# Kernel tuning notes

Measured on AMD Instinct MI355X. Metric: run time of the kernel, lower is better.

The kernel has to match this reference:

```python
import jax, jax.numpy as jnp
import numpy as np

N = 50000
E = 800000
D = 256   # output_channel_dim
K = 32
L = 4     # num_of_layers


def setup_inputs() -> dict:
    key = jax.random.key(0)
    ks = jax.random.split(key, 10)
    x = jax.random.normal(ks[0], (N, 1), dtype=jnp.float32)
    edge_index = jax.random.randint(ks[1], (2, E), 0, N, dtype=jnp.int64)
    edge_attr = jax.random.uniform(ks[2], (E,), dtype=jnp.float32)
    # GGNN per-layer propagation weights (L, D, D)
    weight = jax.random.normal(ks[3], (L, D, D), dtype=jnp.float32) / np.sqrt(D)
    # GRUCell params (torch layout: [r|z|n] stacked along first dim)
    w_ih = jax.random.normal(ks[4], (3 * D, D), dtype=jnp.float32) / np.sqrt(D)
    w_hh = jax.random.normal(ks[5], (3 * D, D), dtype=jnp.float32) / np.sqrt(D)
    b_ih = jax.random.normal(ks[6], (3 * D,), dtype=jnp.float32) * 0.01
    b_hh = jax.random.normal(ks[7], (3 * D,), dtype=jnp.float32) * 0.01
    # readout Linear(D, K)
    w_ro = jax.random.normal(ks[8], (D, K), dtype=jnp.float32) / np.sqrt(D)
    b_ro = jax.random.normal(ks[9], (K,), dtype=jnp.float32) * 0.01
    return {"x": x, "edge_index": edge_index, "edge_attr": edge_attr,
            "weight": weight, "w_ih": w_ih, "w_hh": w_hh,
            "b_ih": b_ih, "b_hh": b_hh, "w_ro": w_ro, "b_ro": b_ro}


def _gru_cell(m, h, w_ih, w_hh, b_ih, b_hh):
    # torch.nn.GRUCell math; gates stacked [r|z|n]
    gi = m @ w_ih.T + b_ih   # (N, 3D)
    gh = h @ w_hh.T + b_hh   # (N, 3D)
    i_r, i_z, i_n = jnp.split(gi, 3, axis=-1)
    h_r, h_z, h_n = jnp.split(gh, 3, axis=-1)
    r = jax.nn.sigmoid(i_r + h_r)
    z = jax.nn.sigmoid(i_z + h_z)
    n = jnp.tanh(i_n + r * h_n)
    return (1.0 - z) * n + z * h


def reference(x, edge_index, edge_attr, weight, w_ih, w_hh, b_ih, b_hh, w_ro, b_ro):
    src, dst = edge_index[0], edge_index[1]
    n_nodes, d = x.shape[0], weight.shape[-1]
    # pad input features with zeros up to out_channels
    h = jnp.concatenate([x, jnp.zeros((n_nodes, d - x.shape[-1]), x.dtype)], axis=-1)
    for i in range(weight.shape[0]):
        m = h @ weight[i]                                    # (N, D)
        msg = edge_attr[:, None] * m[src]                    # (E, D)
        agg = jax.ops.segment_sum(msg, dst, num_segments=n_nodes)  # (N, D)
        h = _gru_cell(agg, h, w_ih, w_hh, b_ih, b_hh)
    logits = h @ w_ro + b_ro                                 # (N, K)
    return jax.nn.softmax(logits, axis=-1)
```

## Files before the change

kernel.cpp:

```cpp
#include <hip/hip_runtime.h>

#define D 256
#define K_OUT 32
#define L_LAYERS 4
#define NPAD 50048

typedef __attribute__((ext_vector_type(8))) short bf16x8;
typedef __attribute__((ext_vector_type(4))) float f32x4;
typedef __attribute__((address_space(3))) unsigned int lds_u32;
typedef const __attribute__((address_space(1))) unsigned int glb_u32;

__device__ __forceinline__ float sigm(float v) { return 1.f / (1.f + __expf(-v)); }
__device__ __forceinline__ unsigned short f2bf(float f) {
    unsigned u = __float_as_uint(f);
    u = u + 0x7fffu + ((u >> 16) & 1u);
    return (unsigned short)(u >> 16);
}
__device__ __forceinline__ float bf2f(unsigned short s) {
    return __uint_as_float(((unsigned)s) << 16);
}
__device__ __forceinline__ void gload16(const unsigned short* g, unsigned short* l) {
    __builtin_amdgcn_global_load_lds((glb_u32*)g, (lds_u32*)l, 16, 0, 0);
}

__device__ __forceinline__ void frag_addr(int f, int bm, int bnd, int lane,
                                          unsigned& off, bool& isA, bool& isG2) {
    if (f < 8) {
        off = (unsigned)(bm + f * 16 + (lane & 15)) * 1024u + ((lane >> 4) << 3);
        isA = true; isG2 = false;
    } else if (f < 16) {
        off = (unsigned)(bm + (f - 8) * 16 + (lane & 15)) * 1024u + 512u + ((lane >> 4) << 3);
        isA = true; isG2 = false;
    } else if (f < 28) {
        int q = f - 16; int gs = q >> 2; int df = q & 3;
        off = (unsigned)(gs * 256 + bnd + df * 16 + (lane & 15)) * 1024u + ((lane >> 4) << 3);
        isA = false; isG2 = (gs == 2);
    } else {
        int q = f - 28; int gs = q >> 2; int df = q & 3;
        off = (unsigned)(gs * 256 + bnd + df * 16 + (lane & 15)) * 1024u + 512u + ((lane >> 4) << 3);
        isA = false; isG2 = (gs == 2);
    }
}

__global__ __launch_bounds__(256) void hist_kernel(const int* __restrict__ dst,
                                                   int* __restrict__ cnt, int E) {
    int idx = blockIdx.x * blockDim.x + threadIdx.x;
    for (int e = idx; e < E; e += gridDim.x * blockDim.x)
        atomicAdd(&cnt[dst[e]], 1);
}

__global__ __launch_bounds__(1024) void scan_kernel(const int* __restrict__ cnt,
                                                    int* __restrict__ rowptr,
                                                    int* __restrict__ cursor, int n) {
    __shared__ int sdata[1024];
    int t = threadIdx.x;
    int chunk = (n + 1023) / 1024;
    int start = t * chunk;
    int end = start + chunk; if (end > n) end = n;
    int s = 0;
    for (int i = start; i < end; i++) s += cnt[i];
    sdata[t] = s;
    __syncthreads();
    for (int off = 1; off < 1024; off <<= 1) {
        int v = (t >= off) ? sdata[t - off] : 0;
        __syncthreads();
        sdata[t] += v;
        __syncthreads();
    }
    int base = sdata[t] - s;
    for (int i = start; i < end; i++) {
        rowptr[i] = base;
        cursor[i] = base;
        base += cnt[i];
    }
    if (end == n && start <= n) rowptr[n] = base;
}

__global__ __launch_bounds__(256) void reorder_kernel(const int* __restrict__ src,
                                                      const int* __restrict__ dst,
                                                      const float* __restrict__ ea,
                                                      int* __restrict__ cursor,
                                                      int* __restrict__ esrc,
                                                      float* __restrict__ eval, int E) {
    int idx = blockIdx.x * blockDim.x + threadIdx.x;
    for (int e = idx; e < E; e += gridDim.x * blockDim.x) {
        int slot = atomicAdd(&cursor[dst[e]], 1);
        esrc[slot] = src[e];
        eval[slot] = ea[e];
    }
}

__global__ __launch_bounds__(256) void prep_wih_kernel(const float* __restrict__ weight,
                                                       const float* __restrict__ w_ih,
                                                       float* __restrict__ P) {
    int l = blockIdx.z;
    const float* A = weight + (size_t)l * D * D;
    float* Cdst = P + (size_t)l * 256 * 768;
    __shared__ float As[32][64 + 4];
    __shared__ float Bs[32][64 + 4];
    int tid = threadIdx.x;
    int tx = tid & 15, ty = tid >> 4;
    int bk = blockIdx.x * 64;
    int bn = blockIdx.y * 64;
    float acc[4][4] = {};
    for (int jb = 0; jb < D; jb += 32) {
        #pragma unroll
        for (int i = 0; i < 2; i++) {
            int lin = tid + i * 256;
            int row = lin >> 3;
            int c4 = (lin & 7) << 2;
            float4 v = *(const float4*)&A[(size_t)(bk + row) * D + jb + c4];
            As[c4+0][row]=v.x; As[c4+1][row]=v.y; As[c4+2][row]=v.z; As[c4+3][row]=v.w;
            float4 w = *(const float4*)&w_ih[(size_t)(bn + row) * D + jb + c4];
            Bs[c4+0][row]=w.x; Bs[c4+1][row]=w.y; Bs[c4+2][row]=w.z; Bs[c4+3][row]=w.w;
        }
        __syncthreads();
        #pragma unroll
        for (int jj = 0; jj < 32; jj++) {
            float a[4], b[4];
            *(float4*)a = *(const float4*)&As[jj][ty*4];
            *(float4*)b = *(const float4*)&Bs[jj][tx*4];
            #pragma unroll
            for (int i = 0; i < 4; i++)
                #pragma unroll
                for (int j = 0; j < 4; j++)
                    acc[i][j] += a[i] * b[j];
        }
        __syncthreads();
    }
    #pragma unroll
    for (int i = 0; i < 4; i++)
        *(float4*)&Cdst[(size_t)(bk + ty*4 + i) * 768 + bn + tx*4] =
            make_float4(acc[i][0], acc[i][1], acc[i][2], acc[i][3]);
}

__global__ __launch_bounds__(256) void pack_bt2_kernel(const float* __restrict__ P,
                                                       const float* __restrict__ w_hh,
                                                       unsigned short* __restrict__ BT2) {
    long long idx = (long long)blockIdx.x * 256 + threadIdx.x;
    int l = (int)(idx >> 20);
    int rem = (int)(idx & 1048575);
    int c = rem >> 10;
    int k2 = rem & 1023;
    int g = c >> 8, d = c & 255;
    int k = k2 & 511;
    float val;
    if (k < 256) {
        val = (g == 0) ? P[(size_t)l * 196608 + (size_t)k * 768 + d]
            : (g == 1) ? P[(size_t)l * 196608 + (size_t)k * 768 + 256 + d]
            : (g == 2) ? P[(size_t)l * 196608 + (size_t)k * 768 + 512 + d]
            : 0.f;
    } else {
        int kk = k - 256;
        val = (g == 0) ? w_hh[(size_t)d * D + kk]
            : (g == 1) ? w_hh[(size_t)(256 + d) * D + kk]
            : (g == 3) ? w_hh[(size_t)(512 + d) * D + kk]
            : 0.f;
    }
    unsigned short hi = f2bf(val);
    BT2[idx] = (k2 < 512) ? hi : f2bf(val - bf2f(hi));
}

__global__ __launch_bounds__(256) void sgather_kernel(const float* __restrict__ x,
                                                      const int* __restrict__ rowptr,
                                                      const int* __restrict__ esrc,
                                                      const float* __restrict__ eval,
                                                      float* __restrict__ sx, int n) {
    int node = blockIdx.x * blockDim.x + threadIdx.x;
    if (node >= n) return;
    float s = 0.f;
    int end = rowptr[node + 1];
    for (int e = rowptr[node]; e < end; e++) s += eval[e] * x[esrc[e]];
    sx[node] = s;
}

__global__ __launch_bounds__(256) void layer0_kernel(const float* __restrict__ x,
                                                     const float* __restrict__ sx,
                                                     const float* __restrict__ P0,
                                                     const float* __restrict__ w_hh,
                                                     const float* __restrict__ b_ih,
                                                     const float* __restrict__ b_hh,
                                                     float* __restrict__ hout, int M) {
    int node = blockIdx.x * 4 + (threadIdx.x >> 6);
    if (node >= M) return;
    int d0 = (threadIdx.x & 63) * 4;
    float sxn = sx[node], xn = x[node];
    float4 r0 = *(const float4*)&P0[d0];
    float4 z0 = *(const float4*)&P0[256 + d0];
    float4 n0 = *(const float4*)&P0[512 + d0];
    float r1[4], z1[4], n1[4];
    #pragma unroll
    for (int j = 0; j < 4; j++) {
        r1[j] = w_hh[(size_t)(d0 + j) * D];
        z1[j] = w_hh[(size_t)(256 + d0 + j) * D];
        n1[j] = w_hh[(size_t)(512 + d0 + j) * D];
    }
    float4 bir = *(const float4*)&b_ih[d0];
    float4 biz = *(const float4*)&b_ih[256 + d0];
    float4 bin = *(const float4*)&b_ih[512 + d0];
    float4 bhr = *(const float4*)&b_hh[d0];
    float4 bhz = *(const float4*)&b_hh[256 + d0];
    float4 bhn = *(const float4*)&b_hh[512 + d0];
    float rr[4] = {sxn*r0.x + xn*r1[0] + bir.x + bhr.x, sxn*r0.y + xn*r1[1] + bir.y + bhr.y,
                   sxn*r0.z + xn*r1[2] + bir.z + bhr.z, sxn*r0.w + xn*r1[3] + bir.w + bhr.w};
    float zz[4] = {sxn*z0.x + xn*z1[0] + biz.x + bhz.x, sxn*z0.y + xn*z1[1] + biz.y + bhz.y,
                   sxn*z0.z + xn*z1[2] + biz.z + bhz.z, sxn*z0.w + xn*z1[3] + biz.w + bhz.w};
    float ni[4] = {sxn*n0.x + bin.x, sxn*n0.y + bin.y, sxn*n0.z + bin.z, sxn*n0.w + bin.w};
    float nh[4] = {xn*n1[0] + bhn.x, xn*n1[1] + bhn.y, xn*n1[2] + bhn.z, xn*n1[3] + bhn.w};
    float o[4];
    #pragma unroll
    for (int j = 0; j < 4; j++) {
        float r = sigm(rr[j]);
        float z = sigm(zz[j]);
        float nn = tanhf(ni[j] + r * nh[j]);
        float hp = (d0 + j == 0) ? xn : 0.f;
        o[j] = (1.f - z) * nn + z * hp;
    }
    *(float4*)&hout[(size_t)node * D + d0] = make_float4(o[0], o[1], o[2], o[3]);
}

__global__ __launch_bounds__(256) void gather_bf_kernel(const float* __restrict__ h,
                                                        const int* __restrict__ rowptr,
                                                        const int* __restrict__ esrc,
                                                        const float* __restrict__ eval,
                                                        unsigned short* __restrict__ A2, int n) {
    int node = (blockIdx.x * 256 + threadIdx.x) >> 6;
    int lane = threadIdx.x & 63;
    if (node >= n) return;
    int beg = rowptr[node], end = rowptr[node + 1];
    float4 acc = make_float4(0.f, 0.f, 0.f, 0.f);
    for (int e = beg; e < end; e++) {
        int s = esrc[e];
        float a = eval[e];
        float4 v = *(const float4*)&h[(size_t)s * D + lane * 4];
        acc.x += a * v.x; acc.y += a * v.y; acc.z += a * v.z; acc.w += a * v.w;
    }
    ushort4 hi = make_ushort4(f2bf(acc.x), f2bf(acc.y), f2bf(acc.z), f2bf(acc.w));
    ushort4 lo = make_ushort4(f2bf(acc.x - bf2f(hi.x)), f2bf(acc.y - bf2f(hi.y)),
                              f2bf(acc.z - bf2f(hi.z)), f2bf(acc.w - bf2f(hi.w)));
    *(ushort4*)&A2[(size_t)node * 1024 + lane * 4] = hi;
    *(ushort4*)&A2[(size_t)node * 1024 + 512 + lane * 4] = lo;
    float4 hv = *(const float4*)&h[(size_t)node * D + lane * 4];
    ushort4 hh = make_ushort4(f2bf(hv.x), f2bf(hv.y), f2bf(hv.z), f2bf(hv.w));
    ushort4 hl = make_ushort4(f2bf(hv.x - bf2f(hh.x)), f2bf(hv.y - bf2f(hh.y)),
                              f2bf(hv.z - bf2f(hh.z)), f2bf(hv.w - bf2f(hh.w)));
    *(ushort4*)&A2[(size_t)node * 1024 + 256 + lane * 4] = hh;
    *(ushort4*)&A2[(size_t)node * 1024 + 768 + lane * 4] = hl;
}

__global__ __launch_bounds__(256, 2) void gru_mfma_kernel(const unsigned short* __restrict__ A2,
                                                          const unsigned short* __restrict__ BT2,
                                                          const float* __restrict__ b_ih,
                                                          const float* __restrict__ b_hh,
                                                          float* __restrict__ h, int M) {
    __shared__ unsigned short sm[2][20480];
    int tid = threadIdx.x;
    int lane = tid & 63;
    int wid = tid >> 6;
    int wr = wid >> 1, wc = wid & 1;

    int bid = blockIdx.x;
    int g, by;
    if (bid < 1536) {
        int ch = bid >> 5;
        int rem = bid & 31;
        g = ch * 8 + (rem & 7);
        by = rem >> 3;
    } else {
        int r = bid - 1536;
        g = 384 + (r >> 2);
        by = r & 3;
    }
    int bm = g * 128;
    int bnd = by * 64;

    unsigned g0off[5], g1off[5];
    int slot0[5], slot1[5];
    bool g0A[5], g0G2[5], g1A[5], g1G2[5];
    #pragma unroll
    for (int i = 0; i < 5; i++) {
        int idx = wid * 5 + i;
        int f0 = (idx < 8) ? idx : idx + 8;
        int f1 = (idx < 8) ? idx + 8 : idx + 20;
        frag_addr(f0, bm, bnd, lane, g0off[i], g0A[i], g0G2[i]);
        frag_addr(f1, bm, bnd, lane, g1off[i], g1A[i], g1G2[i]);
        slot0[i] = f0; slot1[i] = f1;
    }

    f32x4 acc[4][8];
    #pragma unroll
    for (int i = 0; i < 4; i++)
        #pragma unroll
        for (int j = 0; j < 8; j++)
            acc[i][j] = (f32x4){0.f, 0.f, 0.f, 0.f};

    bf16x8 ah[4], al[4], bh[6], bl[6];

#define STAGE_H0(C_, B_)                                                           \
    { _Pragma("unroll")                                                            \
      for (int i = 0; i < 5; i++) {                                                \
        const unsigned short* gp = (g0A[i] ? A2 : BT2) + g0off[i]                  \
            + (C_) * 32 + ((g0G2[i] && (C_) >= 8) ? 262144u : 0u);                 \
        gload16(gp, &sm[B_][slot0[i] * 512]);                                      \
      } }
#define STAGE_H1(C_, B_)                                                           \
    { _Pragma("unroll")                                                            \
      for (int i = 0; i < 5; i++) {                                                \
        const unsigned short* gp = (g1A[i] ? A2 : BT2) + g1off[i]                  \
            + (C_) * 32 + ((g1G2[i] && (C_) >= 8) ? 262144u : 0u);                 \
        gload16(gp, &sm[B_][slot1[i] * 512]);                                      \
      } }

#define KBODY(C_, NIOFF_)                                                          \
    {   int cur = (C_) & 1;                                                        \
        asm volatile("s_waitcnt vmcnt(5)" ::: "memory");                           \
        __builtin_amdgcn_sched_barrier(0);                                         \
        __builtin_amdgcn_s_barrier();                                              \
        if ((C_) < 15) { STAGE_H0((C_) + 1, cur ^ 1); STAGE_H1((C_) + 1, cur ^ 1); } \
        _Pragma("unroll")                                                          \
        for (int m = 0; m < 4; m++)                                                \
            ah[m] = *(const bf16x8*)&sm[cur][(wr * 4 + m) * 512 + lane * 8];       \
        _Pragma("unroll")                                                          \
        for (int j = 0; j < 6; j++) {                                              \
            int fb = 16 + (j >> 1) * 4 + wc * 2 + (j & 1);                         \
            bh[j] = *(const bf16x8*)&sm[cur][fb * 512 + lane * 8];                 \
        }                                                                          \
        _Pragma("unroll")                                                          \
        for (int m = 0; m < 4; m++)                                                \
            _Pragma("unroll")                                                      \
            for (int j = 0; j < 6; j++) {                                          \
                int na = (j < 4) ? j : (NIOFF_) + (j & 1);                         \
                acc[m][na] = __builtin_amdgcn_mfma_f32_16x16x32_bf16(ah[m], bh[j], acc[m][na], 0, 0, 0); \
            }                                                                      \
        if ((C_) < 15) { asm volatile("s_waitcnt vmcnt(10)" ::: "memory"); }       \
        else           { asm volatile("s_waitcnt vmcnt(0)"  ::: "memory"); }       \
        __builtin_amdgcn_sched_barrier(0);                                         \
        __builtin_amdgcn_s_barrier();                                              \
        _Pragma("unroll")                                                          \
        for (int m = 0; m < 4; m++)                                                \
            al[m] = *(const bf16x8*)&sm[cur][(8 + wr * 4 + m) * 512 + lane * 8];   \
        _Pragma("unroll")                                                          \
        for (int j = 0; j < 6; j++) {                                              \
            int fb = 16 + (j >> 1) * 4 + wc * 2 + (j & 1);                         \
            bl[j] = *(const bf16x8*)&sm[cur][(fb + 12) * 512 + lane * 8];          \
        }                                                                          \
        _Pragma("unroll")                                                          \
        for (int m = 0; m < 4; m++)                                                \
            _Pragma("unroll")                                                      \
            for (int j = 0; j < 6; j++) {                                          \
                int na = (j < 4) ? j : (NIOFF_) + (j & 1);                         \
                acc[m][na] = __builtin_amdgcn_mfma_f32_16x16x32_bf16(al[m], bh[j], acc[m][na], 0, 0, 0); \
                acc[m][na] = __builtin_amdgcn_mfma_f32_16x16x32_bf16(ah[m], bl[j], acc[m][na], 0, 0, 0); \
            }                                                                      \
    }

    STAGE_H0(0, 0); STAGE_H1(0, 0);
    KBODY(0, 4)  KBODY(1, 4)  KBODY(2, 4)  KBODY(3, 4)
    KBODY(4, 4)  KBODY(5, 4)  KBODY(6, 4)  KBODY(7, 4)
    KBODY(8, 6)  KBODY(9, 6)  KBODY(10, 6) KBODY(11, 6)
    KBODY(12, 6) KBODY(13, 6) KBODY(14, 6) KBODY(15, 6)
#undef STAGE_H0
#undef STAGE_H1
#undef KBODY

    int rbase = bm + wr * 64 + ((lane >> 4) << 2);
    #pragma unroll
    for (int jj = 0; jj < 2; jj++) {
        int d = bnd + (wc * 2 + jj) * 16 + (lane & 15);
        float cbr = b_ih[d] + b_hh[d];
        float cbz = b_ih[D + d] + b_hh[D + d];
        float bin = b_ih[2 * D + d];
        float bhn = b_hh[2 * D + d];
        #pragma unroll
        for (int m = 0; m < 4; m++) {
            #pragma unroll
            for (int q = 0; q < 4; q++) {
                int row = rbase + m * 16 + q;
                if (row < M) {
                    float r = sigm(acc[m][jj][q] + cbr);
                    float z = sigm(acc[m][2 + jj][q] + cbz);
                    float nn = tanhf(acc[m][4 + jj][q] + bin + r * (acc[m][6 + jj][q] + bhn));
                    float* hp = &h[(size_t)row * D + d];
                    float hv = *hp;
                    *hp = (1.f - z) * nn + z * hv;
                }
            }
        }
    }
}

__global__ __launch_bounds__(256) void readout_kernel(const float* __restrict__ h,
                                                      const float* __restrict__ w_ro,
                                                      const float* __restrict__ b_ro,
                                                      float* __restrict__ out, int M) {
    __shared__ float ws_[D * K_OUT];
    for (int i = threadIdx.x; i < D * K_OUT; i += 256) ws_[i] = w_ro[i];
    __syncthreads();
    int group = threadIdx.x >> 5;
    int col   = threadIdx.x & 31;
    int node  = blockIdx.x * 8 + group;
    if (node >= M) return;
    float a0 = b_ro[col], a1 = 0.f, a2 = 0.f, a3 = 0.f;
    const float* hrow = &h[(size_t)node * D];
    #pragma unroll 4
    for (int k = 0; k < D; k += 4) {
        float4 hv = *(const float4*)&hrow[k];
        a0 += hv.x * ws_[(k + 0) * K_OUT + col];
        a1 += hv.y * ws_[(k + 1) * K_OUT + col];
        a2 += hv.z * ws_[(k + 2) * K_OUT + col];
        a3 += hv.w * ws_[(k + 3) * K_OUT + col];
    }
    float acc = (a0 + a1) + (a2 + a3);
    float mx = acc;
    #pragma unroll
    for (int off = 16; off > 0; off >>= 1) mx = fmaxf(mx, __shfl_xor(mx, off, 32));
    float e = __expf(acc - mx);
    float s = e;
    #pragma unroll
    for (int off = 16; off > 0; off >>= 1) s += __shfl_xor(s, off, 32);
    out[(size_t)node * K_OUT + col] = e / s;
}

extern "C" void kernel_launch(void* const* d_in, const int* in_sizes, int n_in,
                              void* d_out, int out_size, void* d_ws, size_t ws_size,
                              hipStream_t stream) {
    const float* x      = (const float*)d_in[0];
    const int*   ei     = (const int*)d_in[1];
    const float* ea     = (const float*)d_in[2];
    const float* weight = (const float*)d_in[3];
    const float* w_ih   = (const float*)d_in[4];
    const float* w_hh   = (const float*)d_in[5];
    const float* b_ih   = (const float*)d_in[6];
    const float* b_hh   = (const float*)d_in[7];
    const float* w_ro   = (const float*)d_in[8];
    const float* b_ro   = (const float*)d_in[9];
    float* out = (float*)d_out;

    int N = in_sizes[0];
    int E = in_sizes[2];
    const int* src = ei;
    const int* dst = ei + E;

    size_t ND = (size_t)N * D;
    float* h = (float*)d_ws;
    unsigned short* A2 = (unsigned short*)(h + ND);
    float* P = (float*)(A2 + (size_t)NPAD * 1024);
    unsigned short* BT2 = (unsigned short*)(P + (size_t)L_LAYERS * 256 * 768);
    float* sx = (float*)(BT2 + (size_t)L_LAYERS * 1024 * 1024);
    int* cnt = (int*)(sx + N);
    int* rowptr = cnt + (N + 1);
    int* cursor = rowptr + (N + 1);
    int* esrc = cursor + (N + 1);
    float* eval = (float*)(esrc + E);

    hipMemsetAsync(cnt, 0, (N + 1) * sizeof(int), stream);
    hist_kernel<<<1024, 256, 0, stream>>>(dst, cnt, E);
    scan_kernel<<<1, 1024, 0, stream>>>(cnt, rowptr, cursor, N);
    reorder_kernel<<<1024, 256, 0, stream>>>(src, dst, ea, cursor, esrc, eval, E);

    prep_wih_kernel<<<dim3(4, 12, 4), 256, 0, stream>>>(weight, w_ih, P);
    pack_bt2_kernel<<<16384, 256, 0, stream>>>(P, w_hh, BT2);

    sgather_kernel<<<(N + 255) / 256, 256, 0, stream>>>(x, rowptr, esrc, eval, sx, N);
    layer0_kernel<<<(N + 3) / 4, 256, 0, stream>>>(x, sx, P, w_hh, b_ih, b_hh, h, N);

    int nb = (NPAD / 128) * 4;
    int gather_blocks = (N * 64 + 255) / 256;
    for (int l = 1; l < L_LAYERS; l++) {
        gather_bf_kernel<<<gather_blocks, 256, 0, stream>>>(h, rowptr, esrc, eval, A2, N);
        gru_mfma_kernel<<<nb, 256, 0, stream>>>(A2, BT2 + (size_t)l * 1024 * 1024,
                                                b_ih, b_hh, h, N);
    }
    readout_kernel<<<(N + 7) / 8, 256, 0, stream>>>(h, w_ro, b_ro, out, N);
}
```

Baseline: 1.411 ms.

## Single-buffer GRU MFMA kernel for higher occupancy and unroll gather by two edges

The GRU GEMM kernel drops its hand-tuned LDS double buffer and split hi/lo waits for a single buffer that is staged, synchronized and consumed each K chunk. This halves LDS use so launch bounds can ask for 4 blocks per CU, relying on extra waves rather than in-block prefetch to hide load latency. It also raises wave priority around the MFMA block. Separately, the gather kernel processes two edges per iteration with two accumulators to get more loads in flight. The risk is that losing the explicit overlap between loads and compute is not fully made up by the added occupancy, and register limits at 4 blocks per CU may cause spills.

Measured after the change: 3.758 ms. 2.66x slower.

```diff
diff --git a/kernel.cpp b/kernel.cpp
--- a/kernel.cpp
+++ b/kernel.cpp
@@ -228,13 +228,24 @@
     int lane = threadIdx.x & 63;
     if (node >= n) return;
     int beg = rowptr[node], end = rowptr[node + 1];
-    float4 acc = make_float4(0.f, 0.f, 0.f, 0.f);
-    for (int e = beg; e < end; e++) {
-        int s = esrc[e];
-        float a = eval[e];
-        float4 v = *(const float4*)&h[(size_t)s * D + lane * 4];
-        acc.x += a * v.x; acc.y += a * v.y; acc.z += a * v.z; acc.w += a * v.w;
-    }
+    float4 acc0 = make_float4(0.f, 0.f, 0.f, 0.f);
+    float4 acc1 = make_float4(0.f, 0.f, 0.f, 0.f);
+    int e = beg;
+    for (; e + 1 < end; e += 2) {
+        int s0 = esrc[e], s1 = esrc[e + 1];
+        float a0 = eval[e], a1 = eval[e + 1];
+        float4 v0 = *(const float4*)&h[(size_t)s0 * D + lane * 4];
+        float4 v1 = *(const float4*)&h[(size_t)s1 * D + lane * 4];
+        acc0.x += a0 * v0.x; acc0.y += a0 * v0.y; acc0.z += a0 * v0.z; acc0.w += a0 * v0.w;
+        acc1.x += a1 * v1.x; acc1.y += a1 * v1.y; acc1.z += a1 * v1.z; acc1.w += a1 * v1.w;
+    }
+    if (e < end) {
+        int s0 = esrc[e];
+        float a0 = eval[e];
+        float4 v0 = *(const float4*)&h[(size_t)s0 * D + lane * 4];
+        acc0.x += a0 * v0.x; acc0.y += a0 * v0.y; acc0.z += a0 * v0.z; acc0.w += a0 * v0.w;
+    }
+    float4 acc = make_float4(acc0.x + acc1.x, acc0.y + acc1.y, acc0.z + acc1.z, acc0.w + acc1.w);
     ushort4 hi = make_ushort4(f2bf(acc.x), f2bf(acc.y), f2bf(acc.z), f2bf(acc.w));
     ushort4 lo = make_ushort4(f2bf(acc.x - bf2f(hi.x)), f2bf(acc.y - bf2f(hi.y)),
                               f2bf(acc.z - bf2f(hi.z)), f2bf(acc.w - bf2f(hi.w)));
@@ -248,12 +259,12 @@
     *(ushort4*)&A2[(size_t)node * 1024 + 768 + lane * 4] = hl;
 }
 
-__global__ __launch_bounds__(256, 2) void gru_mfma_kernel(const unsigned short* __restrict__ A2,
+__global__ __launch_bounds__(256, 4) void gru_mfma_kernel(const unsigned short* __restrict__ A2,
                                                           const unsigned short* __restrict__ BT2,
                                                           const float* __restrict__ b_ih,
                                                           const float* __restrict__ b_hh,
                                                           float* __restrict__ h, int M) {
-    __shared__ unsigned short sm[2][20480];
+    __shared__ unsigned short sm[20480];
     int tid = threadIdx.x;
     int lane = tid & 63;
     int wid = tid >> 6;
@@ -274,17 +285,12 @@
     int bm = g * 128;
     int bnd = by * 64;
 
-    unsigned g0off[5], g1off[5];
-    int slot0[5], slot1[5];
-    bool g0A[5], g0G2[5], g1A[5], g1G2[5];
-    #pragma unroll
-    for (int i = 0; i < 5; i++) {
-        int idx = wid * 5 + i;
-        int f0 = (idx < 8) ? idx : idx + 8;
-        int f1 = (idx < 8) ? idx + 8 : idx + 20;
-        frag_addr(f0, bm, bnd, lane, g0off[i], g0A[i], g0G2[i]);
-        frag_addr(f1, bm, bnd, lane, g1off[i], g1A[i], g1G2[i]);
-        slot0[i] = f0; slot1[i] = f1;
+    unsigned gbase[10];
+    bool gA[10], gG2[10];
+    #pragma unroll
+    for (int ff = 0; ff < 10; ff++) {
+        int f = wid * 10 + ff;
+        frag_addr(f, bm, bnd, lane, gbase[ff], gA[ff], gG2[ff]);
     }
 
     f32x4 acc[4][8];
@@ -294,73 +300,48 @@
         for (int j = 0; j < 8; j++)
             acc[i][j] = (f32x4){0.f, 0.f, 0.f, 0.f};
 
-    bf16x8 ah[4], al[4], bh[6], bl[6];
-
-#define STAGE_H0(C_, B_)                                                           \
+#define STAGE(C_)                                                                  \
     { _Pragma("unroll")                                                            \
-      for (int i = 0; i < 5; i++) {                                                \
-        const unsigned short* gp = (g0A[i] ? A2 : BT2) + g0off[i]                  \
-            + (C_) * 32 + ((g0G2[i] && (C_) >= 8) ? 262144u : 0u);                 \
-        gload16(gp, &sm[B_][slot0[i] * 512]);                                      \
+      for (int ff = 0; ff < 10; ff++) {                                            \
+        const unsigned short* gp = (gA[ff] ? A2 : BT2) + gbase[ff]                 \
+            + (C_) * 32 + ((gG2[ff] && (C_) >= 8) ? 262144u : 0u);                 \
+        gload16(gp, &sm[(wid * 10 + ff) * 512]);                                   \
       } }
-#define STAGE_H1(C_, B_)                                                           \
-    { _Pragma("unroll")                                                            \
-      for (int i = 0; i < 5; i++) {                                                \
-        const unsigned short* gp = (g1A[i] ? A2 : BT2) + g1off[i]                  \
-            + (C_) * 32 + ((g1G2[i] && (C_) >= 8) ? 262144u : 0u);                 \
-        gload16(gp, &sm[B_][slot1[i] * 512]);                                      \
-      } }
 
 #define KBODY(C_, NIOFF_)                                                          \
-    {   int cur = (C_) & 1;                                                        \
-        asm volatile("s_waitcnt vmcnt(5)" ::: "memory");                           \
-        __builtin_amdgcn_sched_barrier(0);                                         \
-        __builtin_amdgcn_s_barrier();                                              \
-        if ((C_) < 15) { STAGE_H0((C_) + 1, cur ^ 1); STAGE_H1((C_) + 1, cur ^ 1); } \
+    {   STAGE(C_)                                                                  \
+        __syncthreads();                                                           \
+        bf16x8 ah[4], al[4], bh[6], bl[6];                                         \
         _Pragma("unroll")                                                          \
-        for (int m = 0; m < 4; m++)                                                \
-            ah[m] = *(const bf16x8*)&sm[cur][(wr * 4 + m) * 512 + lane * 8];       \
+        for (int m = 0; m < 4; m++) {                                              \
+            ah[m] = *(const bf16x8*)&sm[(wr * 4 + m) * 512 + lane * 8];            \
+            al[m] = *(const bf16x8*)&sm[(8 + wr * 4 + m) * 512 + lane * 8];        \
+        }                                                                          \
         _Pragma("unroll")                                                          \
         for (int j = 0; j < 6; j++) {                                              \
             int fb = 16 + (j >> 1) * 4 + wc * 2 + (j & 1);                         \
-            bh[j] = *(const bf16x8*)&sm[cur][fb * 512 + lane * 8];                 \
+            bh[j] = *(const bf16x8*)&sm[fb * 512 + lane * 8];                      \
+            bl[j] = *(const bf16x8*)&sm[(fb + 12) * 512 + lane * 8];               \
         }                                                                          \
+        __builtin_amdgcn_s_setprio(1);                                             \
         _Pragma("unroll")                                                          \
         for (int m = 0; m < 4; m++)                                                \
             _Pragma("unroll")                                                      \
             for (int j = 0; j < 6; j++) {                                          \
                 int na = (j < 4) ? j : (NIOFF_) + (j & 1);                         \
                 acc[m][na] = __builtin_amdgcn_mfma_f32_16x16x32_bf16(ah[m], bh[j], acc[m][na], 0, 0, 0); \
-            }                                                                      \
-        if ((C_) < 15) { asm volatile("s_waitcnt vmcnt(10)" ::: "memory"); }       \
-        else           { asm volatile("s_waitcnt vmcnt(0)"  ::: "memory"); }       \
-        __builtin_amdgcn_sched_barrier(0);                                         \
-        __builtin_amdgcn_s_barrier();                                              \
-        _Pragma("unroll")                                                          \
-        for (int m = 0; m < 4; m++)                                                \
-            al[m] = *(const bf16x8*)&sm[cur][(8 + wr * 4 + m) * 512 + lane * 8];   \
-        _Pragma("unroll")                                                          \
-        for (int j = 0; j < 6; j++) {                                              \
-            int fb = 16 + (j >> 1) * 4 + wc * 2 + (j & 1);                         \
-            bl[j] = *(const bf16x8*)&sm[cur][(fb + 12) * 512 + lane * 8];          \
-        }                                                                          \
-        _Pragma("unroll")                                                          \
-        for (int m = 0; m < 4; m++)                                                \
-            _Pragma("unroll")                                                      \
-            for (int j = 0; j < 6; j++) {                                          \
-                int na = (j < 4) ? j : (NIOFF_) + (j & 1);                         \
                 acc[m][na] = __builtin_amdgcn_mfma_f32_16x16x32_bf16(al[m], bh[j], acc[m][na], 0, 0, 0); \
                 acc[m][na] = __builtin_amdgcn_mfma_f32_16x16x32_bf16(ah[m], bl[j], acc[m][na], 0, 0, 0); \
             }                                                                      \
-    }
-
-    STAGE_H0(0, 0); STAGE_H1(0, 0);
+        __builtin_amdgcn_s_setprio(0);                                             \
+        __syncthreads();                                                           \
+    }
+
     KBODY(0, 4)  KBODY(1, 4)  KBODY(2, 4)  KBODY(3, 4)
     KBODY(4, 4)  KBODY(5, 4)  KBODY(6, 4)  KBODY(7, 4)
     KBODY(8, 6)  KBODY(9, 6)  KBODY(10, 6) KBODY(11, 6)
     KBODY(12, 6) KBODY(13, 6) KBODY(14, 6) KBODY(15, 6)
-#undef STAGE_H0
-#undef STAGE_H1
+#undef STAGE
 #undef KBODY
 
     int rbase = bm + wr * 64 + ((lane >> 4) << 2);
```
